# Kernel optimization log

Measured on AMD Instinct MI355X. Metric: run time of the kernel, lower is better.

## Reference

```python
import jax, jax.numpy as jnp
import numpy as np

B, S, E = 2, 2048, 2048
H, G = 32, 8          # n_heads, n_groups
D = E // H            # head_dim = 64


def setup_inputs() -> dict:
    key = jax.random.key(0)
    ks = jax.random.split(key, 5)
    scale = 1.0 / np.sqrt(E)
    return {
        "X": jax.random.normal(ks[0], (B, S, E), dtype=jnp.float32),
        "Wq": jax.random.normal(ks[1], (E, E), dtype=jnp.float32) * scale,
        "Wk": jax.random.normal(ks[2], (E, G * D), dtype=jnp.float32) * scale,
        "Wv": jax.random.normal(ks[3], (E, G * D), dtype=jnp.float32) * scale,
        "Wo": jax.random.normal(ks[4], (E, E), dtype=jnp.float32) * scale,
    }


def reference(X, Wq, Wk, Wv, Wo):
    b, s, e = X.shape
    # projections
    q = (X @ Wq).reshape(b, s, H, D).transpose(0, 2, 1, 3)      # [B,H,S,D]
    k = (X @ Wk).reshape(b, s, G, D).transpose(0, 2, 1, 3)      # [B,G,S,D]
    v = (X @ Wv).reshape(b, s, G, D).transpose(0, 2, 1, 3)      # [B,G,S,D]
    # torch view(B, H//G, G, S, D): head h -> (a=h//G, g=h%G)
    q = q.reshape(b, H // G, G, s, D)                           # [B,A,G,S,D]
    scores = jnp.einsum('bagsd,bgtd->bagst', q, k) / np.sqrt(D) # [B,A,G,S,S]
    causal = jnp.tril(jnp.ones((s, s), dtype=bool))
    scores = jnp.where(causal, scores, -jnp.inf)
    probs = jax.nn.softmax(scores, axis=-1)
    out = jnp.einsum('bagst,bgtd->bagsd', probs, v)             # [B,A,G,S,D]
    out = out.reshape(b, H, s, D).transpose(0, 2, 1, 3).reshape(b, s, e)
    return out @ Wo
```

## Files before the change

### kernel.cpp

```cpp
#include <hip/hip_runtime.h>
#include <hip/hip_bf16.h>

typedef unsigned short u16;
typedef __bf16 bf16x8 __attribute__((ext_vector_type(8)));
typedef float f32x4 __attribute__((ext_vector_type(4)));
typedef unsigned short u16x4 __attribute__((ext_vector_type(4)));

#define MFMA16(a, b, c) __builtin_amdgcn_mfma_f32_16x16x32_bf16(a, b, c, 0, 0, 0)

__device__ __forceinline__ u16 f2bf(float f) {
  union { float f; unsigned u; } v; v.f = f;
  unsigned r = v.u + 0x7FFFu + ((v.u >> 16) & 1u);
  return (u16)(r >> 16);
}

__device__ __forceinline__ u16 f2bf_native(float f) {
  __hip_bfloat16 hb = __float2bfloat16(f);
  u16 out;
  __builtin_memcpy(&out, &hb, 2);
  return out;
}

__device__ __forceinline__ void gload16(const u16* g, u16* l) {
  __builtin_amdgcn_global_load_lds(
      (const __attribute__((address_space(1))) unsigned int*)g,
      (__attribute__((address_space(3))) unsigned int*)l, 16, 0, 0);
}

__global__ void cvt_x(const float* __restrict__ X, u16* __restrict__ Xb, int n4) {
  int i = blockIdx.x * blockDim.x + threadIdx.x;
  if (i < n4) {
    float4 v = ((const float4*)X)[i];
    u16x4 o = { f2bf(v.x), f2bf(v.y), f2bf(v.z), f2bf(v.w) };
    ((u16x4*)Xb)[i] = o;
  }
}

__global__ void transpose_cvt(const float* __restrict__ W, u16* __restrict__ WT, int K, int N) {
  __shared__ float t[32][33];
  int n0 = blockIdx.x * 32, k0 = blockIdx.y * 32;
  int tx = threadIdx.x, ty = threadIdx.y;
  t[ty][tx] = W[(size_t)(k0 + ty) * N + n0 + tx];
  __syncthreads();
  WT[(size_t)(n0 + ty) * K + k0 + tx] = f2bf(t[tx][ty]);
}

__device__ __forceinline__ void stage_mat(const u16* __restrict__ src, u16* lds,
                                          int base, int K, int k0, int tid) {
#pragma unroll
  for (int i = 0; i < 4; ++i) {
    int s = i * 512 + tid;
    int row = s >> 3;
    int c = (s & 7) ^ (row & 7);
    gload16(src + (size_t)(base + row) * K + k0 + c * 8, lds + s * 8);
  }
}

template <int STORE>
__global__ __launch_bounds__(512) void gemm256(const u16* __restrict__ A,
                                               const u16* __restrict__ BT,
                                               void* __restrict__ Cv,
                                               int M, int N, int K) {
  __shared__ u16 lA[2][256 * 64];
  __shared__ u16 lB[2][256 * 64];
  const int tid = threadIdx.x;
  const int lane = tid & 63, wave = tid >> 6;
  const int gx = gridDim.x;
  const int nwg = gx * gridDim.y;
  const int bid = blockIdx.y * gx + blockIdx.x;
  const int sw = (bid & 7) * (nwg >> 3) + (bid >> 3);
  const int bx = sw % gx, by = sw / gx;
  const int bm = by * 256, bn = bx * 256;
  const int wr = wave >> 2, wc = wave & 3;
  const int l15 = lane & 15, l4 = lane >> 4;

  f32x4 acc[8][4] = {};

  stage_mat(A,  lA[0], bm, K, 0,  tid);
  stage_mat(BT, lB[0], bn, K, 0,  tid);
  stage_mat(A,  lA[1], bm, K, 64, tid);
  stage_mat(BT, lB[1], bn, K, 64, tid);

  const int NPAIR = K >> 7;
#pragma unroll 1
  for (int pr = 0; pr < NPAIR; ++pr) {
#pragma unroll
    for (int th = 0; th < 2; ++th) {
      const u16* Ar = lA[th];
      const u16* Br = lB[th];
      const int kbase = (pr << 7) + (th << 6);
      bf16x8 bfr[4][2];
#pragma unroll
      for (int q = 0; q < 4; ++q) {
        if (q == 0) {
          asm volatile("s_waitcnt vmcnt(0)" ::: "memory");
          __builtin_amdgcn_s_barrier();
        }
        if (q == 0) {
#pragma unroll
          for (int j = 0; j < 4; ++j) {
            int n = wc * 64 + j * 16 + l15;
#pragma unroll
            for (int kk = 0; kk < 2; ++kk)
              bfr[j][kk] = *(const bf16x8*)&Br[(n * 8 + ((kk * 4 + l4) ^ (n & 7))) * 8];
          }
        }
        bf16x8 af[2][2];
#pragma unroll
        for (int i16 = 0; i16 < 2; ++i16) {
          int r = wr * 128 + q * 32 + i16 * 16 + l15;
#pragma unroll
          for (int kk = 0; kk < 2; ++kk)
            af[i16][kk] = *(const bf16x8*)&Ar[(r * 8 + ((kk * 4 + l4) ^ (r & 7))) * 8];
        }
        if (th == 0 && pr >= 1 && q < 2) {
          if (q == 0) stage_mat(A,  lA[1], bm, K, kbase + 64, tid);
          else        stage_mat(BT, lB[1], bn, K, kbase + 64, tid);
        }
        if (th == 1 && pr + 1 < NPAIR && q < 2) {
          if (q == 0) stage_mat(A,  lA[0], bm, K, kbase + 64, tid);
          else        stage_mat(BT, lB[0], bn, K, kbase + 64, tid);
        }
        __builtin_amdgcn_s_barrier();
        __builtin_amdgcn_s_setprio(1);
#pragma unroll
        for (int i16 = 0; i16 < 2; ++i16)
#pragma unroll
          for (int j = 0; j < 4; ++j)
#pragma unroll
            for (int kk = 0; kk < 2; ++kk)
              acc[q * 2 + i16][j] = MFMA16(af[i16][kk], bfr[j][kk], acc[q * 2 + i16][j]);
        __builtin_amdgcn_s_setprio(0);
        __builtin_amdgcn_s_barrier();
      }
    }
  }

#pragma unroll
  for (int i = 0; i < 8; ++i) {
    int row = bm + wr * 128 + i * 16 + l4 * 4;
#pragma unroll
    for (int j = 0; j < 4; ++j) {
      int col = bn + wc * 64 + j * 16 + l15;
#pragma unroll
      for (int e = 0; e < 4; ++e) {
        float v = acc[i][j][e];
        if (STORE == 2) {
          ((float*)Cv)[(size_t)(row + e) * N + col] = v;
        } else {
          u16* Qb = (u16*)Cv;
          u16* Kb = Qb + 8388608;
          u16* Vt = Kb + 2097152;
          if (col < 2048)       Qb[(size_t)(row + e) * 2048 + col] = f2bf(v * 0.125f);
          else if (col < 2560)  Kb[(size_t)(row + e) * 512 + (col - 2048)] = f2bf(v);
          else                  Vt[(size_t)(col - 2560) * 4096 + (row + e)] = f2bf(v);
        }
      }
    }
  }
}

__global__ __launch_bounds__(512) void attn_fwd(const u16* __restrict__ Q,
                                                const u16* __restrict__ Kb,
                                                const u16* __restrict__ VT,
                                                u16* __restrict__ AO) {
  const int pair = blockIdx.x, g = blockIdx.y, b = blockIdx.z;
  const int tid = threadIdx.x;
  const int lane = tid & 63;
  const int wave = tid >> 6;
  const int a = wave >> 1;
  const int h = a * 8 + g;
  const int l15 = lane & 15, l4 = lane >> 4;

  __shared__ u16 Klds[2][64 * 64];
  __shared__ u16 Vlds[2][64 * 64];
  __shared__ u16 Plds[8][16 * 64];

  const int srow = tid >> 3, sc = (tid & 7) ^ (srow & 7);

  int cur = 0;
#pragma unroll 1
  for (int pass = 0; pass < 2; ++pass) {
    const int qt = (pass == 0) ? pair : 63 - pair;
    const int qw0 = qt * 32 + (wave & 1) * 16;
    const int nt = qt / 2 + 1;

    const u16* qp = Q + (size_t)(b * 2048 + qw0 + l15) * 2048 + h * 64 + l4 * 8;
    bf16x8 qf0 = *(const bf16x8*)qp;
    bf16x8 qf1 = *(const bf16x8*)(qp + 32);

    float m_r = -1e30f, l_r = 0.f;
    f32x4 o[4] = {};

    {
      gload16(Kb + (size_t)(b * 2048 + 0 + srow) * 512 + g * 64 + sc * 8, &Klds[cur][tid * 8]);
      gload16(VT + (size_t)(g * 64 + srow) * 4096 + b * 2048 + 0 + sc * 8, &Vlds[cur][tid * 8]);
      asm volatile("s_waitcnt vmcnt(0)" ::: "memory");
      __builtin_amdgcn_s_barrier();
    }

#pragma unroll 1
    for (int ti = 0; ti < nt; ++ti) {
      const int t0 = ti * 64;
      if (ti + 1 < nt) {
        const int tn = t0 + 64;
        gload16(Kb + (size_t)(b * 2048 + tn + srow) * 512 + g * 64 + sc * 8, &Klds[cur ^ 1][tid * 8]);
        gload16(VT + (size_t)(g * 64 + srow) * 4096 + b * 2048 + tn + sc * 8, &Vlds[cur ^ 1][tid * 8]);
      }

      if (t0 <= qw0 + 15) {
        const u16* Kc = Klds[cur];
        const u16* Vc = Vlds[cur];
        f32x4 s[4];
        __builtin_amdgcn_s_setprio(1);
#pragma unroll
        for (int ct = 0; ct < 4; ++ct) {
          int t = ct * 16 + l15;
          bf16x8 kf0 = *(const bf16x8*)&Kc[(t * 8 + (l4 ^ (t & 7))) * 8];
          bf16x8 kf1 = *(const bf16x8*)&Kc[(t * 8 + ((l4 + 4) ^ (t & 7))) * 8];
          f32x4 sv = {0.f, 0.f, 0.f, 0.f};
          sv = MFMA16(kf0, qf0, sv);
          sv = MFMA16(kf1, qf1, sv);
          s[ct] = sv;
        }
        __builtin_amdgcn_s_setprio(0);

        if (t0 + 63 > qw0) {
          const int qg = qw0 + l15;
#pragma unroll
          for (int ct = 0; ct < 4; ++ct)
#pragma unroll
            for (int e = 0; e < 4; ++e) {
              int tg = t0 + ct * 16 + l4 * 4 + e;
              if (tg > qg) s[ct][e] = -1e30f;
            }
        }

        float m0 = fmaxf(fmaxf(s[0][0], s[0][1]), fmaxf(s[0][2], s[0][3]));
        float m1 = fmaxf(fmaxf(s[1][0], s[1][1]), fmaxf(s[1][2], s[1][3]));
        float m2 = fmaxf(fmaxf(s[2][0], s[2][1]), fmaxf(s[2][2], s[2][3]));
        float m3 = fmaxf(fmaxf(s[3][0], s[3][1]), fmaxf(s[3][2], s[3][3]));
        float mt = fmaxf(fmaxf(m0, m1), fmaxf(m2, m3));
        mt = fmaxf(mt, __shfl_xor(mt, 16));
        mt = fmaxf(mt, __shfl_xor(mt, 32));

        if (!__all(mt <= m_r + 8.0f)) {
          float mn = fmaxf(m_r, mt);
          float alpha = __expf(m_r - mn);
          m_r = mn;
          l_r *= alpha;
#pragma unroll
          for (int e = 0; e < 4; ++e) {
            float ae = __shfl(alpha, l4 * 4 + e);
            o[0][e] *= ae; o[1][e] *= ae; o[2][e] *= ae; o[3][e] *= ae;
          }
        }

        u16* P = Plds[wave];
        float rs = 0.f;
#pragma unroll
        for (int ct = 0; ct < 4; ++ct) {
          u16x4 pk;
#pragma unroll
          for (int e = 0; e < 4; ++e) {
            float p = __expf(s[ct][e] - m_r);
            rs += p;
            pk[e] = f2bf_native(p);
          }
          int slot = (ct * 2 + (l4 >> 1)) ^ (l15 & 7);
          *(u16x4*)&P[l15 * 64 + slot * 8 + (l4 & 1) * 4] = pk;
        }
        rs += __shfl_xor(rs, 16);
        rs += __shfl_xor(rs, 32);
        l_r += rs;

        __builtin_amdgcn_s_setprio(1);
#pragma unroll
        for (int kk = 0; kk < 2; ++kk) {
          bf16x8 pf = *(const bf16x8*)&P[l15 * 64 + (((kk * 4 + l4) ^ (l15 & 7)) * 8)];
#pragma unroll
          for (int cd = 0; cd < 4; ++cd) {
            int d = cd * 16 + l15;
            bf16x8 vf = *(const bf16x8*)&Vc[(d * 8 + ((kk * 4 + l4) ^ (d & 7))) * 8];
            o[cd] = MFMA16(pf, vf, o[cd]);
          }
        }
        __builtin_amdgcn_s_setprio(0);
      }

      asm volatile("s_waitcnt vmcnt(0)" ::: "memory");
      __builtin_amdgcn_s_barrier();
      cur ^= 1;
    }

    float rli = 1.0f / l_r;
#pragma unroll
    for (int cd = 0; cd < 4; ++cd)
#pragma unroll
      for (int e = 0; e < 4; ++e) {
        float rle = __shfl(rli, l4 * 4 + e);
        int r = l4 * 4 + e;
        int d = cd * 16 + l15;
        AO[(size_t)(b * 2048 + qw0 + r) * 2048 + h * 64 + d] = f2bf_native(o[cd][e] * rle);
      }
  }
}

extern "C" void kernel_launch(void* const* d_in, const int* in_sizes, int n_in,
                              void* d_out, int out_size, void* d_ws, size_t ws_size,
                              hipStream_t stream) {
  const float* X  = (const float*)d_in[0];
  const float* Wq = (const float*)d_in[1];
  const float* Wk = (const float*)d_in[2];
  const float* Wv = (const float*)d_in[3];
  const float* Wo = (const float*)d_in[4];
  float* out = (float*)d_out;

  u16* ws  = (u16*)d_ws;
  u16* Xb  = ws;
  u16* WqT = Xb  + 8388608;
  u16* WkT = WqT + 4194304;
  u16* WvT = WkT + 1048576;
  u16* WoT = WvT + 1048576;
  u16* Qb  = WoT + 4194304;
  u16* Kbf = Qb  + 8388608;
  u16* VTb = Kbf + 2097152;
  u16* AOb = Xb;

  cvt_x<<<8192, 256, 0, stream>>>(X, Xb, 2097152);
  dim3 tb(32, 32);
  transpose_cvt<<<dim3(64, 64), tb, 0, stream>>>(Wq, WqT, 2048, 2048);
  transpose_cvt<<<dim3(16, 64), tb, 0, stream>>>(Wk, WkT, 2048, 512);
  transpose_cvt<<<dim3(16, 64), tb, 0, stream>>>(Wv, WvT, 2048, 512);
  transpose_cvt<<<dim3(64, 64), tb, 0, stream>>>(Wo, WoT, 2048, 2048);

  gemm256<4><<<dim3(12, 16), 512, 0, stream>>>(Xb, WqT, Qb, 4096, 3072, 2048);

  attn_fwd<<<dim3(32, 8, 2), 512, 0, stream>>>(Qb, Kbf, VTb, AOb);

  gemm256<2><<<dim3(8, 16), 512, 0, stream>>>(AOb, WoT, out, 4096, 2048, 2048);
}
```

Before: 233.8 us.

## Stage GEMM tiles in quarter chunks with per-wave partial vmcnt waits

Reworks the bf16 GEMM double-buffer pipeline. The next K-tile is now loaded one tile ahead, split into four half-matrix chunks (A-lo, B-lo, B-hi, A-hi) issued across the four q sub-steps. Each wave then waits only until the chunks its rows and columns need have arrived, using vmcnt(4), vmcnt(2) or vmcnt(0). The aim is to spread global-to-LDS traffic evenly and cut stall time at the tile boundary. In exchange, the prefetch distance is shorter than before, and the barrier right after the wait may still serialize the waves.

Result: slower. 247.0 us (+5.7%).

```diff
diff --git a/kernel.cpp b/kernel.cpp
--- a/kernel.cpp
+++ b/kernel.cpp
@@ -45,11 +45,11 @@
   WT[(size_t)(n0 + ty) * K + k0 + tx] = f2bf(t[tx][ty]);
 }
 
-__device__ __forceinline__ void stage_mat(const u16* __restrict__ src, u16* lds,
-                                          int base, int K, int k0, int tid) {
-#pragma unroll
-  for (int i = 0; i < 4; ++i) {
-    int s = i * 512 + tid;
+__device__ __forceinline__ void stage_half(const u16* __restrict__ src, u16* lds,
+                                           int base, int K, int k0, int tid, int half) {
+#pragma unroll
+  for (int i = 0; i < 2; ++i) {
+    int s = half * 1024 + i * 512 + tid;
     int row = s >> 3;
     int c = (s & 7) ^ (row & 7);
     gload16(src + (size_t)(base + row) * K + k0 + c * 8, lds + s * 8);
@@ -72,37 +72,46 @@
   const int bx = sw % gx, by = sw / gx;
   const int bm = by * 256, bn = bx * 256;
   const int wr = wave >> 2, wc = wave & 3;
+  const int bc = wc >> 1;
   const int l15 = lane & 15, l4 = lane >> 4;
 
   f32x4 acc[8][4] = {};
 
-  stage_mat(A,  lA[0], bm, K, 0,  tid);
-  stage_mat(BT, lB[0], bn, K, 0,  tid);
-  stage_mat(A,  lA[1], bm, K, 64, tid);
-  stage_mat(BT, lB[1], bn, K, 64, tid);
+  stage_half(A,  lA[0], bm, K, 0, tid, 0);
+  stage_half(BT, lB[0], bn, K, 0, tid, 0);
+  stage_half(BT, lB[0], bn, K, 0, tid, 1);
+  stage_half(A,  lA[0], bm, K, 0, tid, 1);
 
   const int NPAIR = K >> 7;
 #pragma unroll 1
-  for (int pr = 0; pr < NPAIR; ++pr) {
+  for (int j = 0; j < NPAIR; ++j) {
 #pragma unroll
     for (int th = 0; th < 2; ++th) {
       const u16* Ar = lA[th];
       const u16* Br = lB[th];
-      const int kbase = (pr << 7) + (th << 6);
+      u16* As = lA[th ^ 1];
+      u16* Bs = lB[th ^ 1];
+      const int ks = (j << 7) + ((th + 1) << 6);
+      const bool do_stage = (th == 0) || (j + 1 < NPAIR);
       bf16x8 bfr[4][2];
 #pragma unroll
       for (int q = 0; q < 4; ++q) {
         if (q == 0) {
-          asm volatile("s_waitcnt vmcnt(0)" ::: "memory");
+          if (wr == 0) {
+            if (bc == 0) asm volatile("s_waitcnt vmcnt(4)" ::: "memory");
+            else         asm volatile("s_waitcnt vmcnt(2)" ::: "memory");
+          } else {
+            asm volatile("s_waitcnt vmcnt(0)" ::: "memory");
+          }
           __builtin_amdgcn_s_barrier();
         }
         if (q == 0) {
 #pragma unroll
-          for (int j = 0; j < 4; ++j) {
-            int n = wc * 64 + j * 16 + l15;
+          for (int jj = 0; jj < 4; ++jj) {
+            int n = wc * 64 + jj * 16 + l15;
 #pragma unroll
             for (int kk = 0; kk < 2; ++kk)
-              bfr[j][kk] = *(const bf16x8*)&Br[(n * 8 + ((kk * 4 + l4) ^ (n & 7))) * 8];
+              bfr[jj][kk] = *(const bf16x8*)&Br[(n * 8 + ((kk * 4 + l4) ^ (n & 7))) * 8];
           }
         }
         bf16x8 af[2][2];
@@ -113,23 +122,21 @@
           for (int kk = 0; kk < 2; ++kk)
             af[i16][kk] = *(const bf16x8*)&Ar[(r * 8 + ((kk * 4 + l4) ^ (r & 7))) * 8];
         }
-        if (th == 0 && pr >= 1 && q < 2) {
-          if (q == 0) stage_mat(A,  lA[1], bm, K, kbase + 64, tid);
-          else        stage_mat(BT, lB[1], bn, K, kbase + 64, tid);
-        }
-        if (th == 1 && pr + 1 < NPAIR && q < 2) {
-          if (q == 0) stage_mat(A,  lA[0], bm, K, kbase + 64, tid);
-          else        stage_mat(BT, lB[0], bn, K, kbase + 64, tid);
+        if (do_stage) {
+          if (q == 0)      stage_half(A,  As, bm, K, ks, tid, 0);
+          else if (q == 1) stage_half(BT, Bs, bn, K, ks, tid, 0);
+          else if (q == 2) stage_half(BT, Bs, bn, K, ks, tid, 1);
+          else             stage_half(A,  As, bm, K, ks, tid, 1);
         }
         __builtin_amdgcn_s_barrier();
         __builtin_amdgcn_s_setprio(1);
 #pragma unroll
         for (int i16 = 0; i16 < 2; ++i16)
 #pragma unroll
-          for (int j = 0; j < 4; ++j)
+          for (int jj = 0; jj < 4; ++jj)
 #pragma unroll
             for (int kk = 0; kk < 2; ++kk)
-              acc[q * 2 + i16][j] = MFMA16(af[i16][kk], bfr[j][kk], acc[q * 2 + i16][j]);
+              acc[q * 2 + i16][jj] = MFMA16(af[i16][kk], bfr[jj][kk], acc[q * 2 + i16][jj]);
         __builtin_amdgcn_s_setprio(0);
         __builtin_amdgcn_s_barrier();
       }
```
